# Kernel optimization log

Hardware: AMD Instinct MI355X
Metric: run time of the kernel (lower is better)

Reference implementation:

```python
import jax, jax.numpy as jnp
import numpy as np


def setup_inputs() -> dict:
    key = jax.random.key(0)
    kx, ky = jax.random.split(key)
    x = jax.random.normal(kx, (4096, 256), dtype=jnp.float32)
    y = jax.random.normal(ky, (16384, 256), dtype=jnp.float32)
    return {"x": x, "y": y}


def reference(x, y):
    # Original module: scan over rows of x; for each row x_i compute
    #   sqrt(sum((y - x_i)**2, axis=1))  -> stacked to [Nx, Ny].
    # Batched equivalent (single fused pass, no serial scan):
    #   ||x_i - y_j||^2 = ||x_i||^2 + ||y_j||^2 - 2 <x_i, y_j>
    x2 = jnp.sum(x * x, axis=1)                       # [Nx]
    y2 = jnp.sum(y * y, axis=1)                       # [Ny]
    xy = jnp.einsum("nd,md->nm", x, y)               # [Nx, Ny]
    d2 = x2[:, None] + y2[None, :] - 2.0 * xy
    return jnp.sqrt(jnp.maximum(d2, 0.0))            # [Nx, Ny]
```

## Files before the change

### kernel.cpp

```cpp
#include <hip/hip_runtime.h>
#include <hip/hip_bf16.h>


using bf16x8 = __attribute__((ext_vector_type(8))) short;
using f32x4  = __attribute__((ext_vector_type(4))) float;

constexpr int NXR = 4096;
constexpr int NYR = 16384;
constexpr int DD  = 256;

constexpr int BT = 128;
constexpr int BK = 128;

__device__ inline unsigned short f2bf(float f) {
    unsigned int b = __float_as_uint(f);
    b += 0x7FFFu + ((b >> 16) & 1u);
    return (unsigned short)(b >> 16);
}

#define GLDS(gp, lp) __builtin_amdgcn_global_load_lds(                      \
    (const __attribute__((address_space(1))) void*)(gp),                    \
    (__attribute__((address_space(3))) void*)(lp), 16, 0, 0)

__global__ __launch_bounds__(256) void prep_kernel(const float* __restrict__ x,
                                                   const float* __restrict__ y,
                                                   unsigned short* __restrict__ xb,
                                                   unsigned short* __restrict__ yb,
                                                   float* __restrict__ xn,
                                                   float* __restrict__ yn) {
    const int row  = blockIdx.x * 4 + (threadIdx.x >> 6);
    const int lane = threadIdx.x & 63;
    const bool isx = row < NXR;
    const int r    = isx ? row : row - NXR;
    const float* src = (isx ? x : y) + (size_t)r * DD;
    float4 v = *(const float4*)(src + lane * 4);
    ushort4 u = { f2bf(v.x), f2bf(v.y), f2bf(v.z), f2bf(v.w) };
    unsigned short* dst = (isx ? xb : yb) + (size_t)r * DD;
    *(ushort4*)(dst + lane * 4) = u;
    float s = v.x * v.x + v.y * v.y + v.z * v.z + v.w * v.w;
    #pragma unroll
    for (int off = 32; off > 0; off >>= 1) s += __shfl_down(s, off, 64);
    if (lane == 0) { if (isx) xn[r] = s; else yn[r] = s; }
}

__global__ __launch_bounds__(512) void dist_kernel(const unsigned short* __restrict__ xb,
                                                   const unsigned short* __restrict__ yb,
                                                   const float* __restrict__ xn,
                                                   const float* __restrict__ yn,
                                                   float* __restrict__ out) {
    __shared__ unsigned short lY[BT * BK];
    __shared__ unsigned short lX[BT * BK];

    const int bm = blockIdx.x;
    const int bn = blockIdx.y;
    const int tid  = threadIdx.x;
    const int wave = tid >> 6;
    const int lane = tid & 63;
    const int quad = lane >> 4;
    const int l15  = lane & 15;
    const int wm   = wave & 1;
    const int wn   = wave >> 1;

    f32x4 acc[4][2];
    #pragma unroll
    for (int i = 0; i < 4; ++i)
        #pragma unroll
        for (int j = 0; j < 2; ++j)
            acc[i][j] = f32x4{0.f, 0.f, 0.f, 0.f};

    const int srow_in_wave = lane >> 4;
    const int sslot        = lane & 15;

    #pragma unroll
    for (int kt = 0; kt < 2; ++kt) {
        if (kt) __syncthreads();
        #pragma unroll
        for (int p = 0; p < 4; ++p) {
            const int r = p * 32 + wave * 4 + srow_in_wave;
            const int c = sslot ^ (r & 15);
            const size_t goff = (size_t)r * DD + kt * BK + c * 8;
            GLDS(yb + (size_t)(bn * BT) * DD + goff, &lY[(p * 8 + wave) * 512]);
            GLDS(xb + (size_t)(bm * BT) * DD + goff, &lX[(p * 8 + wave) * 512]);
        }
        __syncthreads();

        const int ybase = (wm * 64 + l15) * BK;
        const int xbase = (wn * 32 + l15) * BK;
        #pragma unroll
        for (int kk = 0; kk < 4; ++kk) {
            const int sw = ((kk * 4 + quad) ^ l15) * 8;
            bf16x8 av[4], bv[2];
            #pragma unroll
            for (int i = 0; i < 4; ++i)
                av[i] = *(const bf16x8*)&lY[ybase + i * 16 * BK + sw];
            #pragma unroll
            for (int j = 0; j < 2; ++j)
                bv[j] = *(const bf16x8*)&lX[xbase + j * 16 * BK + sw];
            #pragma unroll
            for (int i = 0; i < 4; ++i)
                #pragma unroll
                for (int j = 0; j < 2; ++j)
                    acc[i][j] = __builtin_amdgcn_mfma_f32_16x16x32_bf16(
                        av[i], bv[j], acc[i][j], 0, 0, 0);
        }
    }

    const int xr0 = bm * BT + wn * 32;
    const int yc0 = bn * BT + wm * 64;
    #pragma unroll
    for (int i = 0; i < 4; ++i) {
        const int ycol = yc0 + i * 16 + quad * 4;
        const f32x4 ynv = *(const f32x4*)&yn[ycol];
        #pragma unroll
        for (int j = 0; j < 2; ++j) {
            const int xrow = xr0 + j * 16 + l15;
            const float xv = xn[xrow];
            f32x4 d;
            #pragma unroll
            for (int r = 0; r < 4; ++r)
                d[r] = sqrtf(fmaxf(xv + ynv[r] - 2.0f * acc[i][j][r], 0.0f));
            *(f32x4*)&out[(size_t)xrow * NYR + ycol] = d;
        }
    }
}

extern "C" void kernel_launch(void* const* d_in, const int* in_sizes, int n_in,
                              void* d_out, int out_size, void* d_ws, size_t ws_size,
                              hipStream_t stream) {
    const float* x = (const float*)d_in[0];
    const float* y = (const float*)d_in[1];
    float* out = (float*)d_out;

    unsigned short* xb = (unsigned short*)d_ws;
    unsigned short* yb = xb + (size_t)NXR * DD;
    float* xn = (float*)(yb + (size_t)NYR * DD);
    float* yn = xn + NXR;

    prep_kernel<<<(NXR + NYR) / 4, 256, 0, stream>>>(x, y, xb, yb, xn, yn);
    dist_kernel<<<dim3(NXR / BT, NYR / BT), 512, 0, stream>>>(xb, yb, xn, yn, out);
}
```

Measured before the change: 335.3 us.

## Drop LDS staging; load bf16 operands directly from global into registers

The distance kernel stops staging X and Y tiles through shared memory and has each wave read its MFMA operand fragments straight from global memory (served by L2/L1). Blocks shrink to 256 threads, with each wave computing a 64x64 output tile with a 4x4 accumulator array, and the two LDS barriers per k-step go away. The epilogue uses the hardware sqrt builtin and nontemporal stores for the large output. This removes LDS traffic and synchronization, but it relies on caches for operand reuse and issues strided 16-byte global loads, which may raise load latency.

Measured after the change: 371.5 us. 10.8% more time.

```diff
diff --git a/kernel.cpp b/kernel.cpp
--- a/kernel.cpp
+++ b/kernel.cpp
@@ -10,17 +10,12 @@
 constexpr int DD  = 256;
 
 constexpr int BT = 128;
-constexpr int BK = 128;
 
 __device__ inline unsigned short f2bf(float f) {
     unsigned int b = __float_as_uint(f);
     b += 0x7FFFu + ((b >> 16) & 1u);
     return (unsigned short)(b >> 16);
 }
-
-#define GLDS(gp, lp) __builtin_amdgcn_global_load_lds(                      \
-    (const __attribute__((address_space(1))) void*)(gp),                    \
-    (__attribute__((address_space(3))) void*)(lp), 16, 0, 0)
 
 __global__ __launch_bounds__(256) void prep_kernel(const float* __restrict__ x,
                                                    const float* __restrict__ y,
@@ -43,14 +38,11 @@
     if (lane == 0) { if (isx) xn[r] = s; else yn[r] = s; }
 }
 
-__global__ __launch_bounds__(512) void dist_kernel(const unsigned short* __restrict__ xb,
-                                                   const unsigned short* __restrict__ yb,
-                                                   const float* __restrict__ xn,
-                                                   const float* __restrict__ yn,
-                                                   float* __restrict__ out) {
-    __shared__ unsigned short lY[BT * BK];
-    __shared__ unsigned short lX[BT * BK];
-
+__global__ __launch_bounds__(256, 4) void dist_kernel(const unsigned short* __restrict__ xb,
+                                                      const unsigned short* __restrict__ yb,
+                                                      const float* __restrict__ xn,
+                                                      const float* __restrict__ yn,
+                                                      float* __restrict__ out) {
     const int bm = blockIdx.x;
     const int bn = blockIdx.y;
     const int tid  = threadIdx.x;
@@ -61,65 +53,50 @@
     const int wm   = wave & 1;
     const int wn   = wave >> 1;
 
-    f32x4 acc[4][2];
+    const int yr0 = bn * BT + wm * 64;
+    const int xr0 = bm * BT + wn * 64;
+
+    f32x4 acc[4][4];
     #pragma unroll
     for (int i = 0; i < 4; ++i)
         #pragma unroll
-        for (int j = 0; j < 2; ++j)
+        for (int j = 0; j < 4; ++j)
             acc[i][j] = f32x4{0.f, 0.f, 0.f, 0.f};
 
-    const int srow_in_wave = lane >> 4;
-    const int sslot        = lane & 15;
+    const unsigned short* ya = yb + (size_t)(yr0 + l15) * DD + quad * 8;
+    const unsigned short* xa = xb + (size_t)(xr0 + l15) * DD + quad * 8;
 
     #pragma unroll
-    for (int kt = 0; kt < 2; ++kt) {
-        if (kt) __syncthreads();
+    for (int kk = 0; kk < 8; ++kk) {
+        const int ko = kk * 32;
+        bf16x8 av[4], bv[4];
         #pragma unroll
-        for (int p = 0; p < 4; ++p) {
-            const int r = p * 32 + wave * 4 + srow_in_wave;
-            const int c = sslot ^ (r & 15);
-            const size_t goff = (size_t)r * DD + kt * BK + c * 8;
-            GLDS(yb + (size_t)(bn * BT) * DD + goff, &lY[(p * 8 + wave) * 512]);
-            GLDS(xb + (size_t)(bm * BT) * DD + goff, &lX[(p * 8 + wave) * 512]);
-        }
-        __syncthreads();
-
-        const int ybase = (wm * 64 + l15) * BK;
-        const int xbase = (wn * 32 + l15) * BK;
+        for (int i = 0; i < 4; ++i)
+            av[i] = *(const bf16x8*)(ya + (size_t)(i * 16) * DD + ko);
         #pragma unroll
-        for (int kk = 0; kk < 4; ++kk) {
-            const int sw = ((kk * 4 + quad) ^ l15) * 8;
-            bf16x8 av[4], bv[2];
+        for (int j = 0; j < 4; ++j)
+            bv[j] = *(const bf16x8*)(xa + (size_t)(j * 16) * DD + ko);
+        #pragma unroll
+        for (int i = 0; i < 4; ++i)
             #pragma unroll
-            for (int i = 0; i < 4; ++i)
-                av[i] = *(const bf16x8*)&lY[ybase + i * 16 * BK + sw];
-            #pragma unroll
-            for (int j = 0; j < 2; ++j)
-                bv[j] = *(const bf16x8*)&lX[xbase + j * 16 * BK + sw];
-            #pragma unroll
-            for (int i = 0; i < 4; ++i)
-                #pragma unroll
-                for (int j = 0; j < 2; ++j)
-                    acc[i][j] = __builtin_amdgcn_mfma_f32_16x16x32_bf16(
-                        av[i], bv[j], acc[i][j], 0, 0, 0);
-        }
+            for (int j = 0; j < 4; ++j)
+                acc[i][j] = __builtin_amdgcn_mfma_f32_16x16x32_bf16(
+                    av[i], bv[j], acc[i][j], 0, 0, 0);
     }
 
-    const int xr0 = bm * BT + wn * 32;
-    const int yc0 = bn * BT + wm * 64;
     #pragma unroll
     for (int i = 0; i < 4; ++i) {
-        const int ycol = yc0 + i * 16 + quad * 4;
+        const int ycol = yr0 + i * 16 + quad * 4;
         const f32x4 ynv = *(const f32x4*)&yn[ycol];
         #pragma unroll
-        for (int j = 0; j < 2; ++j) {
+        for (int j = 0; j < 4; ++j) {
             const int xrow = xr0 + j * 16 + l15;
             const float xv = xn[xrow];
             f32x4 d;
             #pragma unroll
             for (int r = 0; r < 4; ++r)
-                d[r] = sqrtf(fmaxf(xv + ynv[r] - 2.0f * acc[i][j][r], 0.0f));
-            *(f32x4*)&out[(size_t)xrow * NYR + ycol] = d;
+                d[r] = __builtin_amdgcn_sqrtf(fmaxf(xv + ynv[r] - 2.0f * acc[i][j][r], 0.0f));
+            __builtin_nontemporal_store(d, (f32x4*)&out[(size_t)xrow * NYR + ycol]);
         }
     }
 }
@@ -137,5 +114,5 @@
     float* yn = xn + NXR;
 
     prep_kernel<<<(NXR + NYR) / 4, 256, 0, stream>>>(x, y, xb, yb, xn, yn);
-    dist_kernel<<<dim3(NXR / BT, NYR / BT), 512, 0, stream>>>(xb, yb, xn, yn, out);
+    dist_kernel<<<dim3(NXR / BT, NYR / BT), 256, 0, stream>>>(xb, yb, xn, yn, out);
 }
```
